# Performance work log

Hardware: AMD Instinct MI355X
Metric: run time of the kernel (lower is better)

## Reference

```python
import jax, jax.numpy as jnp
import numpy as np


def setup_inputs() -> dict:
    key = jax.random.key(0)
    k1, k2, k3 = jax.random.split(key, 3)
    B, Cout, Cin, H, W = 8, 64, 64, 256, 256
    Wf_rfft = W // 2 + 1
    init_scale = 0.1
    x = jax.random.normal(k1, (B, Cout, H, W), dtype=jnp.float32)
    weight_fft = jax.random.normal(k2, (Cout, Cin, H, Wf_rfft), dtype=jnp.float32) * init_scale
    bias = jax.random.normal(k3, (Cin,), dtype=jnp.float32) * init_scale
    return {"x": x, "weight_fft": weight_fft, "bias": bias}


def reference(x, weight_fft, bias):
    # x: (B, Cout, H, W); weight_fft: (Cout, Cin, Hf, Wf_rfft); bias: (Cin,)
    B, Cout, H, W = x.shape
    _, Cin, Hf, Wf_rfft = weight_fft.shape
    X_fft = jnp.fft.rfft2(x, axes=(2, 3))  # (B, Cout, H, W//2+1) complex
    # Channel contraction over Cout per frequency bin (original code does a
    # broadcast multiply-then-sum; einsum computes identical math without
    # materializing the (B,Cout,Cin,Hf,Wf) intermediate).
    Z_fft = jnp.einsum('bohw,oihw->bihw', X_fft, weight_fft.astype(X_fft.dtype))
    real_Wf = 2 * (Wf_rfft - 1) if Wf_rfft > 1 else 1
    y = jnp.fft.irfft2(Z_fft, s=(Hf, real_Wf), axes=(2, 3))
    y = y[..., :H, :W]
    return y + bias[None, :, None, None]
```

## Files before the change

kernel.cpp:

```cpp
#include <hip/hip_runtime.h>
#include <hip/hip_bf16.h>
#include <math.h>

#define PI_F 3.14159265358979323846f


#define NWACT 15

__device__ __forceinline__ unsigned pack_bf(float re, float im) {
    unsigned ur = __float_as_uint(re);
    unsigned ui = __float_as_uint(im);
    ur = (ur + 0x7fffu + ((ur >> 16) & 1u)) >> 16;
    ui = (ui + 0x7fffu + ((ui >> 16) & 1u)) & 0xffff0000u;
    return ur | ui;
}
__device__ __forceinline__ float2 unpack_bf(unsigned p) {
    return make_float2(__uint_as_float(p << 16),
                       __uint_as_float(p & 0xffff0000u));
}

__device__ __forceinline__ int s2i(int p) { return p ^ (((p >> 4) & 3) << 2); }

__device__ __forceinline__ float2 cadd(float2 a, float2 b){ return make_float2(a.x+b.x, a.y+b.y); }
__device__ __forceinline__ float2 csub(float2 a, float2 b){ return make_float2(a.x-b.x, a.y-b.y); }
__device__ __forceinline__ float2 cmul(float2 a, float2 b){ return make_float2(a.x*b.x-a.y*b.y, a.x*b.y+a.y*b.x); }

template<int SGN>
__device__ __forceinline__ void mk_tw(int jt, float invh, float2& w1, float2& w2) {
    const float th = (SGN < 0 ? -PI_F : PI_F) * (float)jt * invh;
    __sincosf(th, &w1.y, &w1.x);
    __sincosf(0.5f * th, &w2.y, &w2.x);
}

template<int SGN>
__device__ __forceinline__ void quad2(float2& u0, float2& u1, float2& u2, float2& u3,
                                      float2 w1, float2 w2) {
    const float2 t1 = cmul(w1, u1), t3 = cmul(w1, u3);
    const float2 v0 = cadd(u0, t1), v1 = csub(u0, t1);
    const float2 v2 = cadd(u2, t3), v3 = csub(u2, t3);
    const float2 t2 = cmul(w2, v2);
    float2 t4 = cmul(w2, v3);
    t4 = (SGN < 0) ? make_float2(t4.y, -t4.x) : make_float2(-t4.y, t4.x);
    u0 = cadd(v0, t2); u2 = csub(v0, t2);
    u1 = cadd(v1, t4); u3 = csub(v1, t4);
}

template<int SGN>
__device__ __forceinline__ void fft256(float2* w, int j, const float2* tw,
                                       float2& o0, float2& o1, float2& o2, float2& o3) {
    const int r = (int)(__brev((unsigned)j) >> 26);
    float2 u0 = w[s2i(r)], u1 = w[s2i(r + 128)], u2 = w[s2i(r + 64)], u3 = w[s2i(r + 192)];
    __builtin_amdgcn_wave_barrier();
    {
        const float2 v0 = cadd(u0, u1), v1 = csub(u0, u1);
        const float2 v2 = cadd(u2, u3), v3 = csub(u2, u3);
        const float2 t4 = (SGN < 0) ? make_float2(v3.y, -v3.x) : make_float2(-v3.y, v3.x);
        u0 = cadd(v0, v2); u2 = csub(v0, v2);
        u1 = cadd(v1, t4); u3 = csub(v1, t4);
    }
    const int p4 = s2i(4 * j);
    *(float4*)&w[p4]     = make_float4(u0.x, u0.y, u1.x, u1.y);
    *(float4*)&w[p4 + 2] = make_float4(u2.x, u2.y, u3.x, u3.y);
    __builtin_amdgcn_wave_barrier();
    {
        const int p = ((j >> 2) << 4) | (j & 3);
        float2 a0 = w[s2i(p)], a1 = w[s2i(p+4)], a2 = w[s2i(p+8)], a3 = w[s2i(p+12)];
        quad2<SGN>(a0, a1, a2, a3, tw[0], tw[1]);
        w[s2i(p)] = a0; w[s2i(p+4)] = a1; w[s2i(p+8)] = a2; w[s2i(p+12)] = a3;
    }
    __builtin_amdgcn_wave_barrier();
    {
        const int p = ((j >> 4) << 6) | (j & 15);
        float2 a0 = w[s2i(p)], a1 = w[s2i(p+16)], a2 = w[s2i(p+32)], a3 = w[s2i(p+48)];
        quad2<SGN>(a0, a1, a2, a3, tw[2], tw[3]);
        w[s2i(p)] = a0; w[s2i(p+16)] = a1; w[s2i(p+32)] = a2; w[s2i(p+48)] = a3;
    }
    __builtin_amdgcn_wave_barrier();
    {
        float2 a0 = w[s2i(j)], a1 = w[s2i(j+64)], a2 = w[s2i(j+128)], a3 = w[s2i(j+192)];
        quad2<SGN>(a0, a1, a2, a3, tw[4], tw[5]);
        o0 = a0; o1 = a1; o2 = a2; o3 = a3;
    }
}

template<int SGN>
__device__ __forceinline__ void dft4(float2& u0, float2& u1, float2& u2, float2& u3) {
    const float2 t0 = cadd(u0, u2), t1 = csub(u0, u2);
    const float2 t2 = cadd(u1, u3), t3 = csub(u1, u3);
    const float2 t3i = (SGN < 0) ? make_float2(t3.y, -t3.x) : make_float2(-t3.y, t3.x);
    u0 = cadd(t0, t2); u1 = cadd(t1, t3i);
    u2 = csub(t0, t2); u3 = csub(t1, t3i);
}

template<int SGN>
__device__ __forceinline__ void dft16(float2 x[16]) {
#pragma unroll
    for (int b = 0; b < 4; ++b) dft4<SGN>(x[b], x[b+4], x[b+8], x[b+12]);
    const float sg = (SGN < 0) ? -1.0f : 1.0f;
    const float C8 = 0.9238795325112867f, S8 = 0.3826834323650898f, H = 0.7071067811865476f;
    x[5]  = cmul(x[5],  make_float2(C8,  sg*S8));
    x[6]  = cmul(x[6],  make_float2(H,   sg*H));
    x[7]  = cmul(x[7],  make_float2(S8,  sg*C8));
    x[9]  = cmul(x[9],  make_float2(H,   sg*H));
    x[10] = (SGN < 0) ? make_float2(x[10].y, -x[10].x)
                      : make_float2(-x[10].y, x[10].x);
    x[11] = cmul(x[11], make_float2(-H,  sg*H));
    x[13] = cmul(x[13], make_float2(S8,  sg*C8));
    x[14] = cmul(x[14], make_float2(-H,  sg*H));
    x[15] = cmul(x[15], make_float2(-C8, -sg*S8));
#pragma unroll
    for (int k1 = 0; k1 < 4; ++k1) dft4<SGN>(x[4*k1], x[4*k1+1], x[4*k1+2], x[4*k1+3]);
}

template<int SGN>
__device__ __forceinline__ void colfft16(unsigned* __restrict__ S, int l, int c, bool act) {
    float2 x[16];
    if (act) {
#pragma unroll
        for (int r = 0; r < 16; ++r) x[r] = unpack_bf(S[(16*r + l)*129 + c]);
    } else {
#pragma unroll
        for (int r = 0; r < 16; ++r) x[r] = make_float2(0.0f, 0.0f);
    }
    dft16<SGN>(x);
    float2 twl;
    {
        const float th = (SGN < 0 ? -1.0f : 1.0f) * (2.0f * PI_F / 256.0f) * (float)l;
        __sincosf(th, &twl.y, &twl.x);
    }
    float2 t = twl;
#pragma unroll
    for (int kk = 1; kk < 16; ++kk) {
        const int r = 4*(kk & 3) + (kk >> 2);
        x[r] = cmul(x[r], t);
        if (kk < 15) t = cmul(t, twl);
    }
    if (act) {
#pragma unroll
        for (int kk = 0; kk < 16; ++kk) {
            const int r = 4*(kk & 3) + (kk >> 2);
            S[(16*kk + (l ^ kk))*129 + c] = pack_bf(x[r].x, x[r].y);
        }
    }
    __builtin_amdgcn_wave_barrier();
    if (act) {
#pragma unroll
        for (int n2 = 0; n2 < 16; ++n2) x[n2] = unpack_bf(S[(16*l + (n2 ^ l))*129 + c]);
    }
    dft16<SGN>(x);
    if (act) {
#pragma unroll
        for (int r = 0; r < 16; ++r) {
            const int kk = 4*(r & 3) + (r >> 2);
            S[(16*kk + l)*129 + c] = pack_bf(x[r].x, x[r].y);
        }
    }
    __builtin_amdgcn_wave_barrier();
}

#define SMEM_BYTES (132096 + NWACT * 256 * 8)

__global__ __launch_bounds__(1024) void k_fwd2d(const float* __restrict__ x,
                                                unsigned* __restrict__ Xf) {
    extern __shared__ char smem[];
    unsigned* S = (unsigned*)smem;
    float2* w = (float2*)(smem + 132096) + ((threadIdx.x >> 6) << 8);
    const int t = threadIdx.x, f = t >> 6, j = t & 63;
    const int bo = blockIdx.x;
    const float* xi = x + (size_t)bo * 65536;

    float2 tw[6];
    mk_tw<-1>(j & 3,  0.25f,       tw[0], tw[1]);
    mk_tw<-1>(j & 15, 1.0f/16.0f,  tw[2], tw[3]);
    mk_tw<-1>(j,      1.0f/64.0f,  tw[4], tw[5]);

    if (f < NWACT) {
        for (int rp = f; rp < 128; rp += NWACT) {
            const int r1 = rp, r2 = rp + 128;
            const float4 va = ((const float4*)(xi + (r1 << 8)))[j];
            const float4 vb = ((const float4*)(xi + (r2 << 8)))[j];
            const int p4 = s2i(4 * j);
            *(float4*)&w[p4]     = make_float4(va.x, vb.x, va.y, vb.y);
            *(float4*)&w[p4 + 2] = make_float4(va.z, vb.z, va.w, vb.w);
            __builtin_amdgcn_wave_barrier();
            float2 o0, o1, o2, o3;
            fft256<-1>(w, j, tw, o0, o1, o2, o3);
            const int src = (64 - j) & 63;
            float2 P3, P2;
            P3.x = __shfl(o3.x, src); P3.y = __shfl(o3.y, src);
            P2.x = __shfl(o2.x, src); P2.y = __shfl(o2.y, src);
            const float2 Cj = (j == 0) ? make_float2(o0.x, -o0.y)
                                       : make_float2(P3.x, -P3.y);
            const float2 Ck = (j == 0) ? make_float2(P3.x, -P3.y)
                                       : make_float2(P2.x, -P2.y);
            const float2 Aj = make_float2(0.5f * (o0.x + Cj.x), 0.5f * (o0.y + Cj.y));
            const float2 Bj = make_float2(0.5f * (o0.y - Cj.y), -0.5f * (o0.x - Cj.x));
            const float2 Ak = make_float2(0.5f * (o1.x + Ck.x), 0.5f * (o1.y + Ck.y));
            const float2 Bk = make_float2(0.5f * (o1.y - Ck.y), -0.5f * (o1.x - Ck.x));
            S[r1 * 129 + j]      = pack_bf(Aj.x, Aj.y);
            S[r1 * 129 + 64 + j] = pack_bf(Ak.x, Ak.y);
            S[r2 * 129 + j]      = pack_bf(Bj.x, Bj.y);
            S[r2 * 129 + 64 + j] = pack_bf(Bk.x, Bk.y);
            if (j == 0) {
                S[r1 * 129 + 128] = pack_bf(o2.x, 0.0f);
                S[r2 * 129 + 128] = pack_bf(o2.y, 0.0f);
            }
            __builtin_amdgcn_wave_barrier();
        }
    }
    __syncthreads();
    {
        const int g4 = (t >> 4) & 3, l16 = t & 15;
        for (int T = f; T < 33; T += 16) {
            const int cb = (T < 16) ? T : ((T < 32) ? T + 48 : 128);
            const int c = cb + 16 * g4;
            const bool act = (T < 32) || (g4 == 0);
            colfft16<-1>(S, l16, c, act);
        }
    }
    __syncthreads();
    uint4* dst = (uint4*)(Xf + (size_t)bo * 33024);
    const uint4* src4 = (const uint4*)S;
    for (int e = t; e < 8256; e += 1024) dst[e] = src4[e];
}

__global__ __launch_bounds__(256) void k_einsum(unsigned* __restrict__ Xf,
                                                const float* __restrict__ Wt) {
    __shared__ unsigned xs[512][32];
    const int t = threadIdx.x;
    const int bid = blockIdx.x;
    const int nid = (bid & 7) * 129 + (bid >> 3);
    const size_t n0 = (size_t)nid * 32;

#pragma unroll
    for (int k = 0; k < 16; ++k) {
        const int e = t + 256 * k;
        const int pr = e >> 3, q = e & 7;
        const uint4 v = *reinterpret_cast<const uint4*>(
            Xf + (size_t)pr * 33024 + n0 + (q << 2));
        *reinterpret_cast<uint4*>(&xs[pr][q << 2]) = v;
    }
    __syncthreads();

    const int nl = t & 31, j = t >> 5;
    float2 acc[8][8];
#pragma unroll
    for (int r = 0; r < 8; ++r)
#pragma unroll
        for (int b = 0; b < 8; ++b) acc[r][b] = make_float2(0.0f, 0.0f);

    const float* Wb = Wt + n0 + nl;
    auto wload = [&](int o, float (&buf)[8]) {
#pragma unroll
        for (int r = 0; r < 8; ++r)
            buf[r] = __builtin_nontemporal_load(
                Wb + (size_t)((o << 6) | ((r << 3) | j)) * 33024);
    };
    auto fmab = [&](int o, const float (&wc)[8]) {
        float2 xv[8];
#pragma unroll
        for (int b = 0; b < 8; ++b) xv[b] = unpack_bf(xs[(b << 6) | o][nl]);
#pragma unroll
        for (int r = 0; r < 8; ++r)
#pragma unroll
            for (int b = 0; b < 8; ++b) {
                acc[r][b].x += xv[b].x * wc[r];
                acc[r][b].y += xv[b].y * wc[r];
            }
    };

    float wA[8], wB[8];
    wload(0, wA);
    wload(1, wB);
    for (int o = 0; o < 64; o += 2) {
        float wc0[8];
#pragma unroll
        for (int r = 0; r < 8; ++r) wc0[r] = wA[r];
        wload(min(o + 2, 63), wA);
        fmab(o, wc0);
        float wc1[8];
#pragma unroll
        for (int r = 0; r < 8; ++r) wc1[r] = wB[r];
        wload(min(o + 3, 63), wB);
        fmab(o + 1, wc1);
    }

#pragma unroll
    for (int r = 0; r < 8; ++r) {
        const int i = (r << 3) | j;
#pragma unroll
        for (int b = 0; b < 8; ++b) {
            Xf[(size_t)((b << 6) | i) * 33024 + n0 + nl] =
                pack_bf(acc[r][b].x, acc[r][b].y);
        }
    }
}

__global__ __launch_bounds__(1024) void k_inv2d(const unsigned* __restrict__ Xf,
                                                const float* __restrict__ bias,
                                                float* __restrict__ y) {
    extern __shared__ char smem[];
    unsigned* S = (unsigned*)smem;
    float2* w = (float2*)(smem + 132096) + ((threadIdx.x >> 6) << 8);
    const int t = threadIdx.x, f = t >> 6, j = t & 63;
    const int bo = blockIdx.x;
    const float bv = bias[bo & 63];

    float2 tw[6];
    mk_tw<+1>(j & 3,  0.25f,       tw[0], tw[1]);
    mk_tw<+1>(j & 15, 1.0f/16.0f,  tw[2], tw[3]);
    mk_tw<+1>(j,      1.0f/64.0f,  tw[4], tw[5]);

    {
        uint4* s4 = (uint4*)S;
        const uint4* g4p = (const uint4*)(Xf + (size_t)bo * 33024);
        for (int e = t; e < 8256; e += 1024) s4[e] = g4p[e];
    }
    __syncthreads();
    {
        const int g4 = (t >> 4) & 3, l16 = t & 15;
        for (int T = f; T < 33; T += 16) {
            const int cb = (T < 16) ? T : ((T < 32) ? T + 48 : 128);
            const int c = cb + 16 * g4;
            const bool act = (T < 32) || (g4 == 0);
            colfft16<+1>(S, l16, c, act);
        }
    }
    __syncthreads();
    float* yo = y + (size_t)bo * 65536;
    if (f < NWACT) {
        for (int rp = f; rp < 128; rp += NWACT) {
            const int r1 = rp, r2 = rp + 128;
            const unsigned* Sa = S + r1 * 129;
            const unsigned* Sb = S + r2 * 129;
            const float2 A0 = unpack_bf(Sa[j]),      B0 = unpack_bf(Sb[j]);
            const float2 A1 = unpack_bf(Sa[j + 64]), B1 = unpack_bf(Sb[j + 64]);
            const int i2 = (j == 0) ? 128 : 128 - j;
            const float2 A2 = unpack_bf(Sa[i2]),     B2 = unpack_bf(Sb[i2]);
            const float2 A3 = unpack_bf(Sa[64 - j]), B3 = unpack_bf(Sb[64 - j]);
            const float2 z0 = (j == 0)
                ? make_float2(A0.x, B0.x)
                : make_float2(A0.x - B0.y, A0.y + B0.x);
            const float2 z1 = make_float2(A1.x - B1.y, A1.y + B1.x);
            const float2 z2 = (j == 0)
                ? make_float2(A2.x, B2.x)
                : make_float2(A2.x + B2.y, B2.x - A2.y);
            const float2 z3 = make_float2(A3.x + B3.y, B3.x - A3.y);
            w[s2i(j)]       = z0;
            w[s2i(j +  64)] = z1;
            w[s2i(j + 128)] = z2;
            w[s2i(j + 192)] = z3;
            __builtin_amdgcn_wave_barrier();
            float2 o0, o1, o2, o3;
            fft256<+1>(w, j, tw, o0, o1, o2, o3);
            const float sc = 1.0f / 65536.0f;
            float* y1 = yo + (r1 << 8);
            float* y2 = yo + (r2 << 8);
            __builtin_nontemporal_store(o0.x * sc + bv, y1 + j);
            __builtin_nontemporal_store(o1.x * sc + bv, y1 + j + 64);
            __builtin_nontemporal_store(o2.x * sc + bv, y1 + j + 128);
            __builtin_nontemporal_store(o3.x * sc + bv, y1 + j + 192);
            __builtin_nontemporal_store(o0.y * sc + bv, y2 + j);
            __builtin_nontemporal_store(o1.y * sc + bv, y2 + j + 64);
            __builtin_nontemporal_store(o2.y * sc + bv, y2 + j + 128);
            __builtin_nontemporal_store(o3.y * sc + bv, y2 + j + 192);
            __builtin_amdgcn_wave_barrier();
        }
    }
}

extern "C" void kernel_launch(void* const* d_in, const int* in_sizes, int n_in,
                              void* d_out, int out_size, void* d_ws,
                              size_t ws_size, hipStream_t stream) {
    (void)in_sizes; (void)n_in; (void)out_size; (void)ws_size;
    const float* x    = (const float*)d_in[0];
    const float* wfft = (const float*)d_in[1];
    const float* bias = (const float*)d_in[2];
    float* y = (float*)d_out;
    unsigned* Xf = (unsigned*)d_ws;

    hipFuncSetAttribute((const void*)k_fwd2d,
                        hipFuncAttributeMaxDynamicSharedMemorySize, SMEM_BYTES);
    hipFuncSetAttribute((const void*)k_inv2d,
                        hipFuncAttributeMaxDynamicSharedMemorySize, SMEM_BYTES);

    k_fwd2d<<<512, 1024, SMEM_BYTES, stream>>>(x, Xf);
    k_einsum<<<1032, 256, 0, stream>>>(Xf, wfft);
    k_inv2d<<<512, 1024, SMEM_BYTES, stream>>>(Xf, bias, y);
}
```

Measured before the change: 271.3 us.

## Load FFT inputs directly in bit-reversed order into registers, deepen weight prefetch

The 256-point row FFT now takes its first-stage inputs in registers. The forward kernel reads them straight from global memory at bit-reversed indices with nontemporal loads, and the inverse kernel reads them from the packed spectrum at bit-reversed positions, so the LDS write, barrier and read-back before the first radix-4 stage are gone. The channel-mixing kernel's weight prefetch goes from two slots to four, giving the streamed loads more latency hiding. The catch is scattered, uncoalesced global reads in the forward pass and higher register pressure from the extra prefetch buffers.

```diff
diff --git a/kernel.cpp b/kernel.cpp
--- a/kernel.cpp
+++ b/kernel.cpp
@@ -46,11 +46,9 @@
 }
 
 template<int SGN>
-__device__ __forceinline__ void fft256(float2* w, int j, const float2* tw,
-                                       float2& o0, float2& o1, float2& o2, float2& o3) {
-    const int r = (int)(__brev((unsigned)j) >> 26);
-    float2 u0 = w[s2i(r)], u1 = w[s2i(r + 128)], u2 = w[s2i(r + 64)], u3 = w[s2i(r + 192)];
-    __builtin_amdgcn_wave_barrier();
+__device__ __forceinline__ void fft256_reg(float2* w, int j, const float2* tw,
+                                           float2 u0, float2 u1, float2 u2, float2 u3,
+                                           float2& o0, float2& o1, float2& o2, float2& o3) {
     {
         const float2 v0 = cadd(u0, u1), v1 = csub(u0, u1);
         const float2 v2 = cadd(u2, u3), v3 = csub(u2, u3);
@@ -58,6 +56,7 @@
         u0 = cadd(v0, v2); u2 = csub(v0, v2);
         u1 = cadd(v1, t4); u3 = csub(v1, t4);
     }
+    __builtin_amdgcn_wave_barrier();
     const int p4 = s2i(4 * j);
     *(float4*)&w[p4]     = make_float4(u0.x, u0.y, u1.x, u1.y);
     *(float4*)&w[p4 + 2] = make_float4(u2.x, u2.y, u3.x, u3.y);
@@ -174,17 +173,23 @@
     mk_tw<-1>(j & 15, 1.0f/16.0f,  tw[2], tw[3]);
     mk_tw<-1>(j,      1.0f/64.0f,  tw[4], tw[5]);
 
+    const int rbr = (int)(__brev((unsigned)j) >> 26);
+
     if (f < NWACT) {
         for (int rp = f; rp < 128; rp += NWACT) {
             const int r1 = rp, r2 = rp + 128;
-            const float4 va = ((const float4*)(xi + (r1 << 8)))[j];
-            const float4 vb = ((const float4*)(xi + (r2 << 8)))[j];
-            const int p4 = s2i(4 * j);
-            *(float4*)&w[p4]     = make_float4(va.x, vb.x, va.y, vb.y);
-            *(float4*)&w[p4 + 2] = make_float4(va.z, vb.z, va.w, vb.w);
-            __builtin_amdgcn_wave_barrier();
+            const float* x1 = xi + (r1 << 8);
+            const float* x2 = xi + (r2 << 8);
+            const float2 u0 = make_float2(__builtin_nontemporal_load(x1 + rbr),
+                                          __builtin_nontemporal_load(x2 + rbr));
+            const float2 u1 = make_float2(__builtin_nontemporal_load(x1 + rbr + 128),
+                                          __builtin_nontemporal_load(x2 + rbr + 128));
+            const float2 u2 = make_float2(__builtin_nontemporal_load(x1 + rbr + 64),
+                                          __builtin_nontemporal_load(x2 + rbr + 64));
+            const float2 u3 = make_float2(__builtin_nontemporal_load(x1 + rbr + 192),
+                                          __builtin_nontemporal_load(x2 + rbr + 192));
             float2 o0, o1, o2, o3;
-            fft256<-1>(w, j, tw, o0, o1, o2, o3);
+            fft256_reg<-1>(w, j, tw, u0, u1, u2, u3, o0, o1, o2, o3);
             const int src = (64 - j) & 63;
             float2 P3, P2;
             P3.x = __shfl(o3.x, src); P3.y = __shfl(o3.y, src);
@@ -269,20 +274,26 @@
             }
     };
 
-    float wA[8], wB[8];
-    wload(0, wA);
-    wload(1, wB);
-    for (int o = 0; o < 64; o += 2) {
-        float wc0[8];
-#pragma unroll
-        for (int r = 0; r < 8; ++r) wc0[r] = wA[r];
-        wload(min(o + 2, 63), wA);
-        fmab(o, wc0);
-        float wc1[8];
-#pragma unroll
-        for (int r = 0; r < 8; ++r) wc1[r] = wB[r];
-        wload(min(o + 3, 63), wB);
-        fmab(o + 1, wc1);
+    float w0[8], w1[8], w2[8], w3[8];
+    wload(0, w0); wload(1, w1); wload(2, w2); wload(3, w3);
+    for (int o = 0; o < 64; o += 4) {
+        float c0[8], c1[8], c2[8], c3[8];
+#pragma unroll
+        for (int r = 0; r < 8; ++r) c0[r] = w0[r];
+        wload(min(o + 4, 63), w0);
+        fmab(o, c0);
+#pragma unroll
+        for (int r = 0; r < 8; ++r) c1[r] = w1[r];
+        wload(min(o + 5, 63), w1);
+        fmab(o + 1, c1);
+#pragma unroll
+        for (int r = 0; r < 8; ++r) c2[r] = w2[r];
+        wload(min(o + 6, 63), w2);
+        fmab(o + 2, c2);
+#pragma unroll
+        for (int r = 0; r < 8; ++r) c3[r] = w3[r];
+        wload(min(o + 7, 63), w3);
+        fmab(o + 3, c3);
     }
 
 #pragma unroll
@@ -311,6 +322,8 @@
     mk_tw<+1>(j & 15, 1.0f/16.0f,  tw[2], tw[3]);
     mk_tw<+1>(j,      1.0f/64.0f,  tw[4], tw[5]);
 
+    const int rbr = (int)(__brev((unsigned)j) >> 26);
+
     {
         uint4* s4 = (uint4*)S;
         const uint4* g4p = (const uint4*)(Xf + (size_t)bo * 33024);
@@ -333,26 +346,22 @@
             const int r1 = rp, r2 = rp + 128;
             const unsigned* Sa = S + r1 * 129;
             const unsigned* Sb = S + r2 * 129;
-            const float2 A0 = unpack_bf(Sa[j]),      B0 = unpack_bf(Sb[j]);
-            const float2 A1 = unpack_bf(Sa[j + 64]), B1 = unpack_bf(Sb[j + 64]);
-            const int i2 = (j == 0) ? 128 : 128 - j;
+            const int m = rbr;
+            const float2 A0 = unpack_bf(Sa[m]),      B0 = unpack_bf(Sb[m]);
+            const float2 A1 = unpack_bf(Sa[m + 64]), B1 = unpack_bf(Sb[m + 64]);
+            const int i2 = (m == 0) ? 128 : 128 - m;
             const float2 A2 = unpack_bf(Sa[i2]),     B2 = unpack_bf(Sb[i2]);
-            const float2 A3 = unpack_bf(Sa[64 - j]), B3 = unpack_bf(Sb[64 - j]);
-            const float2 z0 = (j == 0)
+            const float2 A3 = unpack_bf(Sa[64 - m]), B3 = unpack_bf(Sb[64 - m]);
+            const float2 u0 = (m == 0)
                 ? make_float2(A0.x, B0.x)
                 : make_float2(A0.x - B0.y, A0.y + B0.x);
-            const float2 z1 = make_float2(A1.x - B1.y, A1.y + B1.x);
-            const float2 z2 = (j == 0)
+            const float2 u1 = (m == 0)
                 ? make_float2(A2.x, B2.x)
                 : make_float2(A2.x + B2.y, B2.x - A2.y);
-            const float2 z3 = make_float2(A3.x + B3.y, B3.x - A3.y);
-            w[s2i(j)]       = z0;
-            w[s2i(j +  64)] = z1;
-            w[s2i(j + 128)] = z2;
-            w[s2i(j + 192)] = z3;
-            __builtin_amdgcn_wave_barrier();
+            const float2 u2 = make_float2(A1.x - B1.y, A1.y + B1.x);
+            const float2 u3 = make_float2(A3.x + B3.y, B3.x - A3.y);
             float2 o0, o1, o2, o3;
-            fft256<+1>(w, j, tw, o0, o1, o2, o3);
+            fft256_reg<+1>(w, j, tw, u0, u1, u2, u3, o0, o1, o2, o3);
             const float sc = 1.0f / 65536.0f;
             float* y1 = yo + (r1 << 8);
             float* y2 = yo + (r2 << 8);
```

After: 314.2 us. +15.8%, slower.
